# Performance work log

Measured on AMD Instinct MI355X. Metric: run time of the kernel, lower is better.

The kernel has to match this reference:

```python
import jax, jax.numpy as jnp
import numpy as np

DIM = 1024
EPS = 1e-5

def layernorm(x, g, b):
    m = jnp.mean(x, axis=-1, keepdims=True)
    v = jnp.var(x, axis=-1, keepdims=True)
    return (x - m) / jnp.sqrt(v + EPS) * g + b

def setup_inputs() -> dict:
    key = jax.random.key(0)
    ks = jax.random.split(key, 12)
    B, L, D = 4, 2048, DIM
    s = 1.0 / np.sqrt(D)
    return {
        "q": jax.random.normal(ks[0], (B, L, D), jnp.float32),
        "k": jax.random.normal(ks[1], (B, L, D), jnp.float32),
        "v": jax.random.normal(ks[2], (B, L, D), jnp.float32),
        "gq": jnp.ones((D,), jnp.float32), "bq": jnp.zeros((D,), jnp.float32),
        "gk": jnp.ones((D,), jnp.float32), "bk": jnp.zeros((D,), jnp.float32),
        "gv": jnp.ones((D,), jnp.float32), "bv": jnp.zeros((D,), jnp.float32),
        "Wq": jax.random.uniform(ks[3], (D, D), jnp.float32, -s, s),
        "Wk": jax.random.uniform(ks[4], (D, D), jnp.float32, -s, s),
        "Wv": jax.random.uniform(ks[5], (D, D), jnp.float32, -s, s),
        "Wp": jax.random.uniform(ks[6], (D, D), jnp.float32, -s, s),
        "bp": jax.random.uniform(ks[7], (D,), jnp.float32, -s, s),
    }

def reference(q, k, v, gq, bq, gk, bk, gv, bv, Wq, Wk, Wv, Wp, bp):
    scale = DIM ** -0.5
    qn = layernorm(q, gq, bq) @ Wq.T  # [B,Q,D]
    kn = layernorm(k, gk, bk) @ Wk.T  # [B,K,D]
    vn = layernorm(v, gv, bv) @ Wv.T  # [B,K,D]
    attn = jnp.einsum('bqc,bkc->bqk', qn, kn)
    attn = jax.nn.relu(attn) * scale  # ReLU on raw scores, then scale (matches in-place *=)
    attn_mask = jax.nn.softmax(attn, axis=-1)
    out = jnp.einsum('bqk,bkc->bqc', attn_mask, vn)
    out = out @ Wp.T + bp
    return (attn, out)
```

## Files before the change

kernel.cpp:

```cpp
#include <hip/hip_runtime.h>


typedef __attribute__((ext_vector_type(8))) short short8v;
typedef __attribute__((ext_vector_type(4))) float f32x4;

#define DEVI __device__ __forceinline__

DEVI float b2f(unsigned short u) {
  union { unsigned int i; float f; } x;
  x.i = ((unsigned int)u) << 16;
  return x.f;
}
DEVI unsigned short f2b(float f) {
  union { float f; unsigned int i; } x;
  x.f = f;
  unsigned int r = x.i + 0x7fffu + ((x.i >> 16) & 1u);
  return (unsigned short)(r >> 16);
}

DEVI bool sniff_bf16(const unsigned short* wq) {
  int bad = 0;
#pragma unroll
  for (int j = 0; j < 64; ++j) bad |= (fabsf(b2f(wq[j])) > 0.0625f) ? 1 : 0;
  return bad == 0;
}

DEVI void async16(const unsigned short* g, unsigned short* l) {
  __builtin_amdgcn_global_load_lds(
      (const __attribute__((address_space(1))) void*)g,
      (__attribute__((address_space(3))) void*)l, 16, 0, 0);
}

template <int NT>
DEVI void gemm_core(unsigned short* sA, unsigned short* sB,
                    const unsigned short* Ab, const unsigned short* Bb,
                    int m0, int n0, int lda, int ldb, int K, int tid,
                    f32x4 (&acc)[4][NT]) {
  const int BN = NT * 32;
  int lane = tid & 63, w = tid >> 6;
  int l15 = lane & 15, quad = lane >> 4;
  int r8 = lane >> 3;
  int scol = ((lane & 7) ^ r8) * 8;
  const unsigned short* gA = Ab + (size_t)(m0 + w * 32 + r8) * lda + scol;
  const unsigned short* gB = Bb + (size_t)(n0 + w * (BN / 4) + r8) * ldb + scol;
  unsigned short* lA = &sA[(size_t)(w * 32) * 64];
  unsigned short* lB = &sB[(size_t)(w * (BN / 4)) * 64];
  int wm = w & 1, wn = w >> 1;
  int rxor = l15 & 7;
  const unsigned short* rA = &sA[(size_t)(wm * 64 + l15) * 64];
  const unsigned short* rB = &sB[(size_t)(wn * (BN / 2) + l15) * 64];

  for (int k0 = 0; k0 < K; k0 += 64) {
#pragma unroll
    for (int j = 0; j < 4; ++j)
      async16(gA + (size_t)(j * 8) * lda + k0, lA + j * 8 * 64);
#pragma unroll
    for (int j = 0; j < NT; ++j)
      async16(gB + (size_t)(j * 8) * ldb + k0, lB + j * 8 * 64);
    __syncthreads();
#pragma unroll
    for (int c = 0; c < 2; ++c) {
      int col = ((c * 4 + quad) ^ rxor) * 8;
      short8v af[4], bf[NT];
#pragma unroll
      for (int i = 0; i < 4; ++i) af[i] = *(const short8v*)(rA + i * 1024 + col);
#pragma unroll
      for (int i = 0; i < NT; ++i) bf[i] = *(const short8v*)(rB + i * 1024 + col);
#pragma unroll
      for (int mt = 0; mt < 4; ++mt)
#pragma unroll
        for (int nt = 0; nt < NT; ++nt)
          acc[mt][nt] = __builtin_amdgcn_mfma_f32_16x16x32_bf16(af[mt], bf[nt], acc[mt][nt], 0, 0, 0);
    }
    __syncthreads();
  }
}

struct PrepArgs {
  const void* q; const void* k; const void* v;
  const void* g[3]; const void* b[3];
  const void* W[4];
};

__global__ __launch_bounds__(256) void k_prep(PrepArgs pa,
    unsigned short* __restrict__ Wb, unsigned short* __restrict__ XN) {
  bool isbf = sniff_bf16((const unsigned short*)pa.W[0]);
  int bid = blockIdx.x, tid = threadIdx.x;
  if (bid < 2048) {
    int s = bid >> 9;
    size_t inner = ((size_t)(bid & 511)) * 2048 + (size_t)tid * 8;
    unsigned short* dst = Wb + (size_t)s * 1048576 + inner;
    if (isbf) {
      *(uint4*)dst = *(const uint4*)((const unsigned short*)pa.W[s] + inner);
    } else {
      const float* f = (const float*)pa.W[s] + inner;
      float4 a = *(const float4*)f;
      float4 b = *(const float4*)(f + 4);
      ushort4 o0 = { f2b(a.x), f2b(a.y), f2b(a.z), f2b(a.w) };
      ushort4 o1 = { f2b(b.x), f2b(b.y), f2b(b.z), f2b(b.w) };
      *(ushort4*)dst = o0;
      *(ushort4*)(dst + 4) = o1;
    }
  } else {
    int row = bid - 2048;
    int t = row >> 13;
    size_t r = (size_t)(row & 8191);
    const void* src = (t == 0) ? pa.q : (t == 1) ? pa.k : pa.v;
    float x0, x1, x2, x3;
    if (isbf) {
      ushort4 pk = *(const ushort4*)((const unsigned short*)src + r * 1024 + (size_t)tid * 4);
      x0 = b2f(pk.x); x1 = b2f(pk.y); x2 = b2f(pk.z); x3 = b2f(pk.w);
    } else {
      float4 pk = *(const float4*)((const float*)src + r * 1024 + (size_t)tid * 4);
      x0 = pk.x; x1 = pk.y; x2 = pk.z; x3 = pk.w;
    }
    float s1 = x0 + x1 + x2 + x3;
    float s2 = x0 * x0 + x1 * x1 + x2 * x2 + x3 * x3;
    for (int off = 32; off > 0; off >>= 1) {
      s1 += __shfl_down(s1, off);
      s2 += __shfl_down(s2, off);
    }
    __shared__ float sh[8];
    if ((tid & 63) == 0) { sh[tid >> 6] = s1; sh[4 + (tid >> 6)] = s2; }
    __syncthreads();
    float m  = (sh[0] + sh[1] + sh[2] + sh[3]) * (1.0f / 1024.0f);
    float m2 = (sh[4] + sh[5] + sh[6] + sh[7]) * (1.0f / 1024.0f);
    float rstd = rsqrtf(m2 - m * m + 1e-5f);
    float g0, g1, g2, g3, c0, c1, c2, c3;
    if (isbf) {
      ushort4 gv = *(const ushort4*)((const unsigned short*)pa.g[t] + tid * 4);
      ushort4 bb = *(const ushort4*)((const unsigned short*)pa.b[t] + tid * 4);
      g0 = b2f(gv.x); g1 = b2f(gv.y); g2 = b2f(gv.z); g3 = b2f(gv.w);
      c0 = b2f(bb.x); c1 = b2f(bb.y); c2 = b2f(bb.z); c3 = b2f(bb.w);
    } else {
      float4 gv = *(const float4*)((const float*)pa.g[t] + tid * 4);
      float4 bb = *(const float4*)((const float*)pa.b[t] + tid * 4);
      g0 = gv.x; g1 = gv.y; g2 = gv.z; g3 = gv.w;
      c0 = bb.x; c1 = bb.y; c2 = bb.z; c3 = bb.w;
    }
    ushort4 o;
    o.x = f2b((x0 - m) * rstd * g0 + c0);
    o.y = f2b((x1 - m) * rstd * g1 + c1);
    o.z = f2b((x2 - m) * rstd * g2 + c2);
    o.w = f2b((x3 - m) * rstd * g3 + c3);
    *(ushort4*)(XN + (size_t)row * 1024 + (size_t)tid * 4) = o;
  }
}

__global__ __launch_bounds__(256) void k_megaproj(
    const unsigned short* __restrict__ XN, const unsigned short* __restrict__ Wb,
    unsigned short* __restrict__ QN, unsigned short* __restrict__ VNT) {
  __shared__ __align__(16) unsigned short sA[128 * 64];
  __shared__ __align__(16) unsigned short sB[128 * 64];
  int x = blockIdx.x, tid = threadIdx.x;
  int lane = tid & 63, w = tid >> 6;
  int wm = w & 1, wn = w >> 1;
  int l15 = lane & 15, quad = lane >> 4;
  f32x4 acc[4][4];
#pragma unroll
  for (int i = 0; i < 4; ++i)
#pragma unroll
    for (int j = 0; j < 4; ++j) acc[i][j] = (f32x4){0.f, 0.f, 0.f, 0.f};

  if (x < 1024) {
    int t = x >> 9, i = x & 511;
    int m0 = (i >> 3) * 128, n0 = (i & 7) * 128;
    gemm_core<4>(sA, sB, XN + (size_t)t * 8388608, Wb + (size_t)t * 1048576,
                 m0, n0, 1024, 1024, 1024, tid, acc);
    unsigned short* C = QN + (size_t)t * 8388608;
#pragma unroll
    for (int mt = 0; mt < 4; ++mt) {
      int mb = m0 + wm * 64 + mt * 16 + quad * 4;
#pragma unroll
      for (int nt = 0; nt < 4; ++nt) {
        int n = n0 + wn * 64 + nt * 16 + l15;
        f32x4 vc = acc[mt][nt];
#pragma unroll
        for (int r2 = 0; r2 < 4; ++r2) C[(size_t)(mb + r2) * 1024 + n] = f2b(vc[r2]);
      }
    }
  } else {
    int i = x - 1024, z = i >> 7, j = i & 127;
    int m0 = (j >> 3) * 128, n0 = (j & 7) * 128;
    gemm_core<4>(sA, sB, XN + 2 * 8388608 + (size_t)z * 2097152,
                 Wb + 2 * 1048576, m0, n0, 1024, 1024, 1024, tid, acc);
    unsigned short* Ct = VNT + (size_t)z * 2097152;
#pragma unroll
    for (int mt = 0; mt < 4; ++mt) {
      int mb = m0 + wm * 64 + mt * 16 + quad * 4;
#pragma unroll
      for (int nt = 0; nt < 4; ++nt) {
        int n = n0 + wn * 64 + nt * 16 + l15;
        f32x4 vc = acc[mt][nt];
        ushort4 o = { f2b(vc[0]), f2b(vc[1]), f2b(vc[2]), f2b(vc[3]) };
        *(ushort4*)&Ct[(size_t)n * 2048 + mb] = o;
      }
    }
  }
}

template <int EPI, int NT>
__global__ __launch_bounds__(256) void k_gemm(
    const unsigned short* __restrict__ A, const unsigned short* __restrict__ B,
    void* __restrict__ Cv, long long coff,
    int K, int lda, int ldb, int ldc,
    long long sAb, long long sBb, long long sCb,
    float scale, const void* __restrict__ bias,
    const unsigned short* __restrict__ wq_sniff) {
  __shared__ __align__(16) unsigned short sA[128 * 64];
  __shared__ __align__(16) unsigned short sB[NT * 32 * 64];
  const int BN = NT * 32;
  int tid = threadIdx.x;
  int lane = tid & 63, w = tid >> 6;
  int wm = w & 1, wn = w >> 1;
  int l15 = lane & 15, quad = lane >> 4;
  int m0 = blockIdx.y * 128, n0 = blockIdx.x * BN;
  f32x4 acc[4][NT];
#pragma unroll
  for (int i = 0; i < 4; ++i)
#pragma unroll
    for (int j = 0; j < NT; ++j) acc[i][j] = (f32x4){0.f, 0.f, 0.f, 0.f};

  gemm_core<NT>(sA, sB, A + (long long)blockIdx.z * sAb,
                B + (long long)blockIdx.z * sBb, m0, n0, lda, ldb, K, tid, acc);

  long long cbase = coff + (long long)blockIdx.z * sCb;
  bool isbf = (EPI != 0) ? sniff_bf16(wq_sniff) : true;
#pragma unroll
  for (int mt = 0; mt < 4; ++mt) {
    int mb = m0 + wm * 64 + mt * 16 + quad * 4;
#pragma unroll
    for (int nt = 0; nt < NT; ++nt) {
      int n = n0 + wn * (BN / 2) + nt * 16 + l15;
      f32x4 vc = acc[mt][nt];
      if (EPI == 0) {
        unsigned short* C = (unsigned short*)Cv + cbase;
#pragma unroll
        for (int r2 = 0; r2 < 4; ++r2) C[(size_t)(mb + r2) * ldc + n] = f2b(vc[r2]);
      } else if (EPI == 1) {
        if (isbf) {
          unsigned short* C = (unsigned short*)Cv + cbase;
#pragma unroll
          for (int r2 = 0; r2 < 4; ++r2)
            C[(size_t)(mb + r2) * ldc + n] = f2b(fmaxf(vc[r2], 0.f) * scale);
        } else {
          float* C = (float*)Cv + cbase;
#pragma unroll
          for (int r2 = 0; r2 < 4; ++r2)
            C[(size_t)(mb + r2) * ldc + n] = fmaxf(vc[r2], 0.f) * scale;
        }
      } else {
        float bv2 = isbf ? b2f(((const unsigned short*)bias)[n])
                         : ((const float*)bias)[n];
        if (isbf) {
          unsigned short* C = (unsigned short*)Cv + cbase;
#pragma unroll
          for (int r2 = 0; r2 < 4; ++r2) C[(size_t)(mb + r2) * ldc + n] = f2b(vc[r2] + bv2);
        } else {
          float* C = (float*)Cv + cbase;
#pragma unroll
          for (int r2 = 0; r2 < 4; ++r2) C[(size_t)(mb + r2) * ldc + n] = vc[r2] + bv2;
        }
      }
    }
  }
}

__global__ __launch_bounds__(256) void k_softmax(const void* __restrict__ S,
    unsigned short* __restrict__ P, const unsigned short* __restrict__ wq_sniff) {
  bool isbf = sniff_bf16(wq_sniff);
  size_t row = blockIdx.x;
  int tid = threadIdx.x;
  float v[8];
  if (isbf) {
    const unsigned short* s = (const unsigned short*)S + row * 2048 + (size_t)tid * 8;
    ushort4 a = *(const ushort4*)s;
    ushort4 b = *(const ushort4*)(s + 4);
    v[0] = b2f(a.x); v[1] = b2f(a.y); v[2] = b2f(a.z); v[3] = b2f(a.w);
    v[4] = b2f(b.x); v[5] = b2f(b.y); v[6] = b2f(b.z); v[7] = b2f(b.w);
  } else {
    const float* s = (const float*)S + row * 2048 + (size_t)tid * 8;
    float4 a = *(const float4*)s;
    float4 b = *(const float4*)(s + 4);
    v[0] = a.x; v[1] = a.y; v[2] = a.z; v[3] = a.w;
    v[4] = b.x; v[5] = b.y; v[6] = b.z; v[7] = b.w;
  }
  float mx = v[0];
#pragma unroll
  for (int j = 1; j < 8; ++j) mx = fmaxf(mx, v[j]);
  for (int off = 32; off > 0; off >>= 1) mx = fmaxf(mx, __shfl_down(mx, off));
  __shared__ float sh[8];
  if ((tid & 63) == 0) sh[tid >> 6] = mx;
  __syncthreads();
  mx = fmaxf(fmaxf(sh[0], sh[1]), fmaxf(sh[2], sh[3]));
  float sum = 0.f;
#pragma unroll
  for (int j = 0; j < 8; ++j) { v[j] = __expf(v[j] - mx); sum += v[j]; }
  for (int off = 32; off > 0; off >>= 1) sum += __shfl_down(sum, off);
  if ((tid & 63) == 0) sh[4 + (tid >> 6)] = sum;
  __syncthreads();
  float inv = 1.0f / (sh[4] + sh[5] + sh[6] + sh[7]);
  ushort4 o0 = { f2b(v[0] * inv), f2b(v[1] * inv), f2b(v[2] * inv), f2b(v[3] * inv) };
  ushort4 o1 = { f2b(v[4] * inv), f2b(v[5] * inv), f2b(v[6] * inv), f2b(v[7] * inv) };
  unsigned short* p = P + row * 2048 + (size_t)tid * 8;
  *(ushort4*)p = o0;
  *(ushort4*)(p + 4) = o1;
}

static const size_t MB_ = 1024 * 1024;
static const size_t OFF_W   = 0;
static const size_t OFF_XN  = 8 * MB_ + 128 * 1024;
static const size_t OFF_QN  = OFF_XN + 48 * MB_;
static const size_t OFF_VNT = OFF_QN + 32 * MB_;
static const size_t OFF_P   = OFF_XN;
static const size_t OFF_O1  = OFF_XN + 32 * MB_;

extern "C" void kernel_launch(void* const* d_in, const int* in_sizes, int n_in,
                              void* d_out, int out_size, void* d_ws, size_t ws_size,
                              hipStream_t stream) {
  (void)in_sizes; (void)n_in; (void)out_size; (void)ws_size;
  char* ws = (char*)d_ws;
  unsigned short* Wb  = (unsigned short*)(ws + OFF_W);
  unsigned short* XN  = (unsigned short*)(ws + OFF_XN);
  unsigned short* QN  = (unsigned short*)(ws + OFF_QN);
  unsigned short* VNT = (unsigned short*)(ws + OFF_VNT);
  unsigned short* P   = (unsigned short*)(ws + OFF_P);
  unsigned short* O1  = (unsigned short*)(ws + OFF_O1);
  const unsigned short* WqS = (const unsigned short*)d_in[9];

  PrepArgs pa;
  pa.q = d_in[0]; pa.k = d_in[1]; pa.v = d_in[2];
  pa.g[0] = d_in[3]; pa.b[0] = d_in[4];
  pa.g[1] = d_in[5]; pa.b[1] = d_in[6];
  pa.g[2] = d_in[7]; pa.b[2] = d_in[8];
  pa.W[0] = d_in[9]; pa.W[1] = d_in[10]; pa.W[2] = d_in[11]; pa.W[3] = d_in[12];

  k_prep<<<26624, 256, 0, stream>>>(pa, Wb, XN);

  k_megaproj<<<1536, 256, 0, stream>>>(XN, Wb, QN, VNT);

  k_gemm<1, 4><<<dim3(16, 16, 4), 256, 0, stream>>>(
      QN, QN + 8388608, d_out,
      0,
      1024, 1024, 1024, 2048,
      2097152LL, 2097152LL, 4194304LL,
      0.03125f, nullptr, WqS);

  k_softmax<<<8192, 256, 0, stream>>>(d_out, P, WqS);

  k_gemm<0, 2><<<dim3(16, 16, 4), 256, 0, stream>>>(
      P, VNT, O1,
      0,
      2048, 2048, 2048, 1024,
      4194304LL, 2097152LL, 2097152LL,
      0.f, nullptr, WqS);

  k_gemm<3, 4><<<dim3(8, 64, 1), 256, 0, stream>>>(
      O1, Wb + 3 * 1048576, d_out,
      16777216,
      1024, 1024, 1024, 1024,
      0LL, 0LL, 0LL,
      0.f, d_in[13], WqS);
}
```

Measured before the change: 435.5 us.

## Double-buffer GEMM LDS tiles with async prefetch and XCD-aware block swizzle

The GEMM core now keeps two LDS buffers and issues the global-to-LDS async loads for tile t+2 while tile t is being consumed. It uses manual vmcnt waits and raw barriers instead of __syncthreads, and raises wave priority around the MFMA block. Block indices are also remapped so that neighbouring tiles land on the same XCD, which should improve L2 reuse. The cost is doubled LDS per block, which may lower occupancy, and more fragile hand-written synchronisation. The swizzle assumes the block count divides evenly by 8.

```diff
diff --git a/kernel.cpp b/kernel.cpp
--- a/kernel.cpp
+++ b/kernel.cpp
@@ -30,6 +30,13 @@
       (const __attribute__((address_space(1))) void*)g,
       (__attribute__((address_space(3))) void*)l, 16, 0, 0);
 }
+
+DEVI void bar() { asm volatile("s_barrier" ::: "memory"); }
+DEVI void wait_lgkm0() { asm volatile("s_waitcnt lgkmcnt(0)" ::: "memory"); }
+template <int N> DEVI void wait_vm();
+template <> DEVI void wait_vm<0>() { asm volatile("s_waitcnt vmcnt(0)" ::: "memory"); }
+template <> DEVI void wait_vm<6>() { asm volatile("s_waitcnt vmcnt(6)" ::: "memory"); }
+template <> DEVI void wait_vm<8>() { asm volatile("s_waitcnt vmcnt(8)" ::: "memory"); }
 
 template <int NT>
 DEVI void gemm_core(unsigned short* sA, unsigned short* sB,
@@ -37,27 +44,44 @@
                     int m0, int n0, int lda, int ldb, int K, int tid,
                     f32x4 (&acc)[4][NT]) {
   const int BN = NT * 32;
+  const int ASZ = 128 * 64;
+  const int BSZ = BN * 64;
   int lane = tid & 63, w = tid >> 6;
   int l15 = lane & 15, quad = lane >> 4;
   int r8 = lane >> 3;
   int scol = ((lane & 7) ^ r8) * 8;
   const unsigned short* gA = Ab + (size_t)(m0 + w * 32 + r8) * lda + scol;
   const unsigned short* gB = Bb + (size_t)(n0 + w * (BN / 4) + r8) * ldb + scol;
-  unsigned short* lA = &sA[(size_t)(w * 32) * 64];
-  unsigned short* lB = &sB[(size_t)(w * (BN / 4)) * 64];
   int wm = w & 1, wn = w >> 1;
   int rxor = l15 & 7;
-  const unsigned short* rA = &sA[(size_t)(wm * 64 + l15) * 64];
-  const unsigned short* rB = &sB[(size_t)(wn * (BN / 2) + l15) * 64];
-
-  for (int k0 = 0; k0 < K; k0 += 64) {
+  const int nst = K >> 6;
+
+  auto stage = [&](int b, int t) {
+    unsigned short* lA = sA + b * ASZ + (size_t)(w * 32) * 64;
+    unsigned short* lB = sB + b * BSZ + (size_t)(w * (BN / 4)) * 64;
+    int k0 = t << 6;
 #pragma unroll
     for (int j = 0; j < 4; ++j)
       async16(gA + (size_t)(j * 8) * lda + k0, lA + j * 8 * 64);
 #pragma unroll
     for (int j = 0; j < NT; ++j)
       async16(gB + (size_t)(j * 8) * ldb + k0, lB + j * 8 * 64);
-    __syncthreads();
+  };
+
+  stage(0, 0);
+  if (nst > 1) {
+    stage(1, 1);
+    wait_vm<4 + NT>();
+  } else {
+    wait_vm<0>();
+  }
+  __builtin_amdgcn_sched_barrier(0);
+  bar();
+
+  for (int t = 0; t < nst; ++t) {
+    int b = t & 1;
+    const unsigned short* rA = sA + b * ASZ + (size_t)(wm * 64 + l15) * 64;
+    const unsigned short* rB = sB + b * BSZ + (size_t)(wn * (BN / 2) + l15) * 64;
 #pragma unroll
     for (int c = 0; c < 2; ++c) {
       int col = ((c * 4 + quad) ^ rxor) * 8;
@@ -66,15 +90,31 @@
       for (int i = 0; i < 4; ++i) af[i] = *(const short8v*)(rA + i * 1024 + col);
 #pragma unroll
       for (int i = 0; i < NT; ++i) bf[i] = *(const short8v*)(rB + i * 1024 + col);
+      __builtin_amdgcn_s_setprio(1);
 #pragma unroll
       for (int mt = 0; mt < 4; ++mt)
 #pragma unroll
         for (int nt = 0; nt < NT; ++nt)
           acc[mt][nt] = __builtin_amdgcn_mfma_f32_16x16x32_bf16(af[mt], bf[nt], acc[mt][nt], 0, 0, 0);
-    }
-    __syncthreads();
-  }
-}
+      __builtin_amdgcn_s_setprio(0);
+    }
+    if (t + 1 < nst) {
+      wait_lgkm0();
+      __builtin_amdgcn_sched_barrier(0);
+      bar();
+      if (t + 2 < nst) {
+        stage(b, t + 2);
+        wait_vm<4 + NT>();
+      } else {
+        wait_vm<0>();
+      }
+      __builtin_amdgcn_sched_barrier(0);
+      bar();
+    }
+  }
+}
+
+DEVI int xcd_swz(int f, int nb) { return (f & 7) * (nb >> 3) + (f >> 3); }
 
 struct PrepArgs {
   const void* q; const void* k; const void* v;
@@ -150,9 +190,9 @@
 __global__ __launch_bounds__(256) void k_megaproj(
     const unsigned short* __restrict__ XN, const unsigned short* __restrict__ Wb,
     unsigned short* __restrict__ QN, unsigned short* __restrict__ VNT) {
-  __shared__ __align__(16) unsigned short sA[128 * 64];
-  __shared__ __align__(16) unsigned short sB[128 * 64];
-  int x = blockIdx.x, tid = threadIdx.x;
+  __shared__ __align__(16) unsigned short sA[2 * 128 * 64];
+  __shared__ __align__(16) unsigned short sB[2 * 128 * 64];
+  int x = xcd_swz((int)blockIdx.x, 1536), tid = threadIdx.x;
   int lane = tid & 63, w = tid >> 6;
   int wm = w & 1, wn = w >> 1;
   int l15 = lane & 15, quad = lane >> 4;
@@ -207,24 +247,34 @@
     long long sAb, long long sBb, long long sCb,
     float scale, const void* __restrict__ bias,
     const unsigned short* __restrict__ wq_sniff) {
-  __shared__ __align__(16) unsigned short sA[128 * 64];
-  __shared__ __align__(16) unsigned short sB[NT * 32 * 64];
+  __shared__ __align__(16) unsigned short sA[2 * 128 * 64];
+  __shared__ __align__(16) unsigned short sB[2 * NT * 32 * 64];
   const int BN = NT * 32;
   int tid = threadIdx.x;
   int lane = tid & 63, w = tid >> 6;
   int wm = w & 1, wn = w >> 1;
   int l15 = lane & 15, quad = lane >> 4;
-  int m0 = blockIdx.y * 128, n0 = blockIdx.x * BN;
+
+  int gx = gridDim.x, gy = gridDim.y;
+  int nb = gx * gy * (int)gridDim.z;
+  int f = (int)blockIdx.x + gx * ((int)blockIdx.y + gy * (int)blockIdx.z);
+  f = xcd_swz(f, nb);
+  int bx = f % gx;
+  int rem = f / gx;
+  int by = rem % gy;
+  int bz = rem / gy;
+
+  int m0 = by * 128, n0 = bx * BN;
   f32x4 acc[4][NT];
 #pragma unroll
   for (int i = 0; i < 4; ++i)
 #pragma unroll
     for (int j = 0; j < NT; ++j) acc[i][j] = (f32x4){0.f, 0.f, 0.f, 0.f};
 
-  gemm_core<NT>(sA, sB, A + (long long)blockIdx.z * sAb,
-                B + (long long)blockIdx.z * sBb, m0, n0, lda, ldb, K, tid, acc);
-
-  long long cbase = coff + (long long)blockIdx.z * sCb;
+  gemm_core<NT>(sA, sB, A + (long long)bz * sAb,
+                B + (long long)bz * sBb, m0, n0, lda, ldb, K, tid, acc);
+
+  long long cbase = coff + (long long)bz * sCb;
   bool isbf = (EPI != 0) ? sniff_bf16(wq_sniff) : true;
 #pragma unroll
   for (int mt = 0; mt < 4; ++mt) {
```

Result: no change. 428.3 us (-1.6%).
